# Performance work log

Hardware: AMD Instinct MI355X
Metric: run time of the kernel (lower is better)

Reference implementation:

```python
import jax, jax.numpy as jnp
import numpy as np

B, N, E = 4, 10000, 320000
IN_F, ATT_D, H = 256, 256, 8
DK = ATT_D // H  # 32
ALPHA = 0.2      # leaky relu slope
NORM_IDX = 0     # attention_norm_idx


def setup_inputs() -> dict:
    key = jax.random.key(0)
    k1, k2, k3, k4 = jax.random.split(key, 4)
    x = jax.random.normal(k1, (B, N, IN_F), dtype=jnp.float32)
    edge = jax.random.randint(k2, (B, 2, E), 0, N)
    # xavier_normal-ish init
    W = jax.random.normal(k3, (IN_F, ATT_D), dtype=jnp.float32) * (1.414 * np.sqrt(2.0 / (IN_F + ATT_D))).astype(np.float32)
    a = jax.random.normal(k4, (1, 2 * DK, 1, 1), dtype=jnp.float32) * 0.1
    return {"x": x, "edge": edge, "W": W, "a": a}


def reference(x, edge, W, a):
    # wx: [B, N, ATT_D]
    wx = jnp.einsum('bni,io->bno', x, W)
    # h: [B, N, DK, H] (view(B,-1,h,d_k).transpose(2,3))
    h = wx.reshape(B, N, H, DK).transpose(0, 1, 3, 2)
    # a * edge_h summed over the 2*DK dim is linear per endpoint, so
    # precompute per-node scores then gather per edge (same math, no [B,2dk,E,H] tensor).
    a_vec = a[0, :, 0, 0]            # [2*DK]
    a_src, a_dst = a_vec[:DK], a_vec[DK:]
    s_src = jnp.einsum('bnkh,k->bnh', h, a_src)   # [B, N, H]
    s_dst = jnp.einsum('bnkh,k->bnh', h, a_dst)   # [B, N, H]
    src = edge[:, 0, :]  # [B, E]
    dst = edge[:, 1, :]
    e_lin = (jnp.take_along_axis(s_src, src[:, :, None], axis=1)
             + jnp.take_along_axis(s_dst, dst[:, :, None], axis=1))  # [B, E, H]
    edge_e = jnp.where(e_lin >= 0, e_lin, ALPHA * e_lin)  # leaky relu
    # segment softmax grouped by edge[:, NORM_IDX, :], per batch element
    seg = (edge[:, NORM_IDX, :] + jnp.arange(B)[:, None] * N).reshape(-1)  # [B*E]
    scores = edge_e.reshape(B * E, H)
    mx = jax.ops.segment_max(scores, seg, num_segments=B * N)   # [B*N, H]
    ex = jnp.exp(scores - mx[seg])
    denom = jax.ops.segment_sum(ex, seg, num_segments=B * N)
    attention = (ex / (denom[seg] + 1e-16)).reshape(B, E, H)
    return attention, wx
```

## Files before the change

kernel.cpp:

```cpp
#include <hip/hip_runtime.h>
#include <hip/hip_bf16.h>

#define BB 4
#define NN 10000
#define EE 320000
#define HH 8
#define NHQ 2
#define NRQ 2
#define SEGR (NN / NRQ)
#define NSLICE 16
#define ESL (EE / NSLICE)
#define UU 4
#define SCALE 16777216.0f
#define INVSC (1.0f / 16777216.0f)

typedef float f4 __attribute__((ext_vector_type(4)));
typedef short s8v __attribute__((ext_vector_type(8)));
typedef unsigned short u16x8 __attribute__((ext_vector_type(8)));

__device__ __forceinline__ unsigned short f2bf(float f) {
  unsigned int u = __float_as_uint(f);
  u += 0x7FFFu + ((u >> 16) & 1u);
  return (unsigned short)(u >> 16);
}
__device__ __forceinline__ float bf2f(unsigned short s) {
  return __uint_as_float(((unsigned int)s) << 16);
}
__device__ __forceinline__ unsigned int ordf(float f) {
  unsigned int u = __float_as_uint(f);
  return (u & 0x80000000u) ? ~u : (u | 0x80000000u);
}
__device__ __forceinline__ float unordf(unsigned int u) {
  unsigned int b = (u & 0x80000000u) ? (u & 0x7FFFFFFFu) : ~u;
  return __uint_as_float(b);
}

__global__ __launch_bounds__(256) void k_transpose(const float* __restrict__ W,
                                                   unsigned short* __restrict__ Wt,
                                                   unsigned int* __restrict__ mxbuf) {
  if (blockIdx.x == 0 && blockIdx.y == 0 && threadIdx.x < 16) mxbuf[threadIdx.x] = 0u;
  __shared__ float tile[64][65];
  const int n0 = blockIdx.x * 64, k0 = blockIdx.y * 64;
  for (int i = threadIdx.x; i < 4096; i += 256) {
    int kk = i >> 6, nn = i & 63;
    tile[kk][nn] = W[(size_t)(k0 + kk) * 256 + n0 + nn];
  }
  __syncthreads();
  for (int i = threadIdx.x; i < 4096; i += 256) {
    int nn = i >> 6, kk = i & 63;
    Wt[(size_t)(n0 + nn) * 256 + (k0 + kk)] = f2bf(tile[kk][nn]);
  }
}

__global__ __launch_bounds__(256, 2) void k_gemm(const float* __restrict__ x,
                                                 const unsigned short* __restrict__ Wt,
                                                 const float* __restrict__ a,
                                                 float* __restrict__ wx,
                                                 unsigned short* __restrict__ ssbf,
                                                 unsigned short* __restrict__ sdbf,
                                                 unsigned int* __restrict__ mxbuf) {
  __shared__ unsigned short sA[64][40];
  __shared__ unsigned short sB[256][40];
  __shared__ unsigned int lmx[16];
  const int tid = threadIdx.x;
  const int lane = tid & 63;
  const int wv = tid >> 6;
  const int row0 = blockIdx.x << 6;
  const int fr = lane & 15;
  const int fg = lane >> 4;
  f4 acc[4][4] = {};
  const int ar = tid >> 2;
  const int ak = (tid & 3) << 3;
  if (tid < 16) lmx[tid] = 0u;

  for (int k0 = 0; k0 < 256; k0 += 32) {
    const float* xp = x + (size_t)(row0 + ar) * 256 + k0 + ak;
    f4 v0 = *(const f4*)xp;
    f4 v1 = *(const f4*)(xp + 4);
    u16x8 av;
    av[0] = f2bf(v0[0]); av[1] = f2bf(v0[1]); av[2] = f2bf(v0[2]); av[3] = f2bf(v0[3]);
    av[4] = f2bf(v1[0]); av[5] = f2bf(v1[1]); av[6] = f2bf(v1[2]); av[7] = f2bf(v1[3]);
    *(u16x8*)&sA[ar][ak] = av;
#pragma unroll
    for (int j = 0; j < 4; ++j) {
      int ci = tid + (j << 8);
      int col = ci >> 2;
      int ks = (ci & 3) << 3;
      *(u16x8*)&sB[col][ks] = *(const u16x8*)(Wt + (size_t)col * 256 + k0 + ks);
    }
    __syncthreads();
    s8v afr[4], bfr[4];
#pragma unroll
    for (int m = 0; m < 4; ++m) afr[m] = *(const s8v*)&sA[m * 16 + fr][fg << 3];
#pragma unroll
    for (int n = 0; n < 4; ++n) bfr[n] = *(const s8v*)&sB[wv * 64 + n * 16 + fr][fg << 3];
#pragma unroll
    for (int m = 0; m < 4; ++m)
#pragma unroll
      for (int n = 0; n < 4; ++n)
        acc[m][n] = __builtin_amdgcn_mfma_f32_16x16x32_bf16(afr[m], bfr[n], acc[m][n], 0, 0, 0);
    __syncthreads();
  }
#pragma unroll
  for (int m = 0; m < 4; ++m)
#pragma unroll
    for (int n = 0; n < 4; ++n) {
      int col = wv * 64 + n * 16 + fr;
#pragma unroll
      for (int q = 0; q < 4; ++q) {
        int row = row0 + m * 16 + fg * 4 + q;
        wx[(size_t)row * 256 + col] = acc[m][n][q];
      }
    }
  const float as0 = a[fr], as1 = a[16 + fr];
  const float ad0 = a[32 + fr], ad1 = a[48 + fr];
  unsigned mp0 = 0u, mp1 = 0u, md0 = 0u, md1 = 0u;
#pragma unroll
  for (int m = 0; m < 4; ++m)
#pragma unroll
    for (int q = 0; q < 4; ++q) {
      float p0 = acc[m][0][q] * as0 + acc[m][1][q] * as1;
      float p1 = acc[m][2][q] * as0 + acc[m][3][q] * as1;
      float d0 = acc[m][0][q] * ad0 + acc[m][1][q] * ad1;
      float d1 = acc[m][2][q] * ad0 + acc[m][3][q] * ad1;
#pragma unroll
      for (int msk = 1; msk <= 8; msk <<= 1) {
        p0 += __shfl_xor(p0, msk);
        p1 += __shfl_xor(p1, msk);
        d0 += __shfl_xor(d0, msk);
        d1 += __shfl_xor(d1, msk);
      }
      mp0 = max(mp0, ordf(p0)); mp1 = max(mp1, ordf(p1));
      md0 = max(md0, ordf(d0)); md1 = max(md1, ordf(d1));
      if (fr == 0) {
        int row = row0 + m * 16 + fg * 4 + q;
        unsigned sspk = (unsigned)f2bf(p0) | ((unsigned)f2bf(p1) << 16);
        unsigned sdpk = (unsigned)f2bf(d0) | ((unsigned)f2bf(d1) << 16);
        ((unsigned*)ssbf)[(size_t)row * 4 + wv] = sspk;
        ((unsigned*)sdbf)[(size_t)row * 4 + wv] = sdpk;
      }
    }
  if (fr == 0) {
    atomicMax(&lmx[wv * 2],     mp0);
    atomicMax(&lmx[wv * 2 + 1], mp1);
    atomicMax(&lmx[8 + wv * 2],     md0);
    atomicMax(&lmx[8 + wv * 2 + 1], md1);
  }
  __syncthreads();
  if (tid < 16 && lmx[tid]) atomicMax(&mxbuf[tid], lmx[tid]);
}

__global__ __launch_bounds__(1024) void k_bin(const int* __restrict__ edge,
                                              const unsigned short* __restrict__ ssbf,
                                              const unsigned short* __restrict__ sdbf,
                                              const unsigned int* __restrict__ mxbuf,
                                              unsigned int* __restrict__ partial) {
  extern __shared__ unsigned int ldsu[];
  unsigned int* hist = ldsu;
  uint2* stg = (uint2*)(ldsu + 4 * SEGR);
  const int blk = blockIdx.x;
  const int r = blk & (NSLICE - 1);
  const int c = blk / NSLICE;
  const int rq = c & 1;
  const int hq = (c >> 1) & 1;
  const int b = c >> 2;
  const int tid = threadIdx.x;
  const int lo = rq * SEGR;
  for (int i = tid; i < 4 * SEGR; i += 1024) hist[i] = 0u;
  const unsigned short* ssb = ssbf + ((size_t)b * NN + lo) * 8 + hq * 4;
  for (int i = tid; i < SEGR; i += 1024) stg[i] = *(const uint2*)(ssb + (size_t)i * 8);
  __syncthreads();
  float MH[4];
#pragma unroll
  for (int j = 0; j < 4; ++j)
    MH[j] = fmaxf(unordf(mxbuf[hq * 4 + j]) + unordf(mxbuf[8 + hq * 4 + j]), 0.f);
  const int* eps = edge + (size_t)b * 2 * EE + r * ESL;
  const int* epd = eps + EE;
  const unsigned short* sdb = sdbf + (size_t)b * NN * 8 + hq * 4;
  for (int base = 0; base < ESL; base += UU * 1024) {
    int ls4[UU], dst4[UU];
    bool v4[UU];
#pragma unroll
    for (int u = 0; u < UU; ++u) {
      int i = base + tid + u * 1024;
      bool inb = i < ESL;
      int s = inb ? eps[i] : 0;
      dst4[u] = inb ? epd[i] : 0;
      int ls = s - lo;
      v4[u] = inb && ((unsigned)ls < (unsigned)SEGR);
      ls4[u] = ls;
    }
    uint2 du4[UU];
#pragma unroll
    for (int u = 0; u < UU; ++u)
      if (v4[u]) du4[u] = *(const uint2*)(sdb + (size_t)dst4[u] * 8);
#pragma unroll
    for (int u = 0; u < UU; ++u) {
      if (v4[u]) {
        uint2 su = stg[ls4[u]];
        float t0 = __uint_as_float(su.x << 16) + __uint_as_float(du4[u].x << 16);
        float t1 = __uint_as_float(su.x & 0xFFFF0000u) + __uint_as_float(du4[u].x & 0xFFFF0000u);
        float t2 = __uint_as_float(su.y << 16) + __uint_as_float(du4[u].y << 16);
        float t3 = __uint_as_float(su.y & 0xFFFF0000u) + __uint_as_float(du4[u].y & 0xFFFF0000u);
        t0 = t0 >= 0.f ? t0 : 0.2f * t0;
        t1 = t1 >= 0.f ? t1 : 0.2f * t1;
        t2 = t2 >= 0.f ? t2 : 0.2f * t2;
        t3 = t3 >= 0.f ? t3 : 0.2f * t3;
        atomicAdd(&hist[0 * SEGR + ls4[u]], (unsigned)(__expf(t0 - MH[0]) * SCALE + 0.5f));
        atomicAdd(&hist[1 * SEGR + ls4[u]], (unsigned)(__expf(t1 - MH[1]) * SCALE + 0.5f));
        atomicAdd(&hist[2 * SEGR + ls4[u]], (unsigned)(__expf(t2 - MH[2]) * SCALE + 0.5f));
        atomicAdd(&hist[3 * SEGR + ls4[u]], (unsigned)(__expf(t3 - MH[3]) * SCALE + 0.5f));
      }
    }
  }
  __syncthreads();
  f4* pout = (f4*)(partial + (size_t)blk * (4 * SEGR));
  const f4* lin = (const f4*)hist;
  for (int i = tid; i < SEGR; i += 1024) pout[i] = lin[i];
}

__global__ __launch_bounds__(256) void k_reduce(const unsigned int* __restrict__ partial,
                                                unsigned short* __restrict__ dnbf) {
  const int t = blockIdx.x * 256 + threadIdx.x;
  if (t >= BB * NHQ * NRQ * SEGR) return;
  const int ls = t % SEGR;
  const int c = t / SEGR;
  const unsigned int* pp = partial + (size_t)c * NSLICE * (4 * SEGR);
  unsigned long long s[4] = {0, 0, 0, 0};
#pragma unroll 4
  for (int r = 0; r < NSLICE; ++r)
#pragma unroll
    for (int h = 0; h < 4; ++h)
      s[h] += pp[(size_t)r * (4 * SEGR) + h * SEGR + ls];
  const int rq = c & 1, hq = (c >> 1) & 1, b = c >> 2;
  uint2 pk;
  pk.x = (unsigned)f2bf((float)s[0] * INVSC) | ((unsigned)f2bf((float)s[1] * INVSC) << 16);
  pk.y = (unsigned)f2bf((float)s[2] * INVSC) | ((unsigned)f2bf((float)s[3] * INVSC) << 16);
  *(uint2*)(dnbf + ((size_t)b * NN + rq * SEGR + ls) * 8 + hq * 4) = pk;
}

__global__ __launch_bounds__(256) void k_fin(const int* __restrict__ edge,
                                             const unsigned short* __restrict__ ssbf,
                                             const unsigned short* __restrict__ sdbf,
                                             const unsigned short* __restrict__ dnbf,
                                             const unsigned int* __restrict__ mxbuf,
                                             float* __restrict__ att) {
  const int idx = blockIdx.x * 256 + threadIdx.x;
  const int b = idx / EE;
  const int e = idx - b * EE;
  const int src = edge[(size_t)b * 2 * EE + e];
  const int dst = edge[(size_t)b * 2 * EE + EE + e];
  const size_t seg = (size_t)b * NN + src;
  float MM[8];
#pragma unroll
  for (int j = 0; j < 8; ++j)
    MM[j] = fmaxf(unordf(mxbuf[j]) + unordf(mxbuf[8 + j]), 0.f);
  u16x8 ss = *(const u16x8*)(ssbf + seg * 8);
  u16x8 sd = *(const u16x8*)(sdbf + ((size_t)b * NN + dst) * 8);
  u16x8 dn = *(const u16x8*)(dnbf + seg * 8);
  f4 o0, o1;
#pragma unroll
  for (int j = 0; j < 4; ++j) {
    float t0 = bf2f(ss[j]) + bf2f(sd[j]);
    t0 = t0 >= 0.f ? t0 : 0.2f * t0;
    float t1 = bf2f(ss[4 + j]) + bf2f(sd[4 + j]);
    t1 = t1 >= 0.f ? t1 : 0.2f * t1;
    float n0 = __expf(t0 - MM[j]);
    float n1 = __expf(t1 - MM[4 + j]);
    o0[j] = n0 / fmaxf(bf2f(dn[j]), n0);
    o1[j] = n1 / fmaxf(bf2f(dn[4 + j]), n1);
  }
  f4* op = (f4*)(att + (size_t)idx * 8);
  op[0] = o0;
  op[1] = o1;
}

extern "C" void kernel_launch(void* const* d_in, const int* in_sizes, int n_in,
                              void* d_out, int out_size, void* d_ws, size_t ws_size,
                              hipStream_t stream) {
  const float* x = (const float*)d_in[0];
  const int* edge = (const int*)d_in[1];
  const float* W = (const float*)d_in[2];
  const float* a = (const float*)d_in[3];

  float* att = (float*)d_out;
  float* wx = att + (size_t)BB * EE * HH;

  unsigned int* partial = (unsigned int*)att;

  char* ws = (char*)d_ws;
  unsigned short* Wt = (unsigned short*)ws;
  unsigned short* ssbf = (unsigned short*)(ws + 131072);
  unsigned short* sdbf = ssbf + 320000;
  unsigned short* dnbf = sdbf + 320000;
  unsigned int* mxbuf = (unsigned int*)(dnbf + 320000);

  hipFuncSetAttribute((const void*)k_bin, hipFuncAttributeMaxDynamicSharedMemorySize,
                      4 * SEGR * 4 + SEGR * 8);

  k_transpose<<<dim3(4, 4), 256, 0, stream>>>(W, Wt, mxbuf);
  k_gemm<<<625, 256, 0, stream>>>(x, Wt, a, wx, ssbf, sdbf, mxbuf);
  k_bin<<<BB * NHQ * NRQ * NSLICE, 1024, 4 * SEGR * 4 + SEGR * 8, stream>>>(edge, ssbf, sdbf, mxbuf, partial);
  k_reduce<<<(BB * NHQ * NRQ * SEGR + 255) / 256, 256, 0, stream>>>(partial, dnbf);
  k_fin<<<5000, 256, 0, stream>>>(edge, ssbf, sdbf, dnbf, mxbuf, att);
}
```

Baseline: 89.78 us.

## Restructure GEMM: LDS-resident W half per block, per-wave 16-row strips with register A

Result: slower. 93.32 us (+3.9%).

```diff
diff --git a/kernel.cpp b/kernel.cpp
--- a/kernel.cpp
+++ b/kernel.cpp
@@ -52,99 +52,95 @@
   }
 }
 
-__global__ __launch_bounds__(256, 2) void k_gemm(const float* __restrict__ x,
+__global__ __launch_bounds__(512, 4) void k_gemm(const float* __restrict__ x,
                                                  const unsigned short* __restrict__ Wt,
                                                  const float* __restrict__ a,
                                                  float* __restrict__ wx,
                                                  unsigned short* __restrict__ ssbf,
                                                  unsigned short* __restrict__ sdbf,
                                                  unsigned int* __restrict__ mxbuf) {
-  __shared__ unsigned short sA[64][40];
-  __shared__ unsigned short sB[256][40];
-  __shared__ unsigned int lmx[16];
+  extern __shared__ char dyn[];
+  unsigned short (*sB)[256] = (unsigned short(*)[256])dyn;
+  unsigned int* lmx = (unsigned int*)(dyn + 128 * 256 * 2);
   const int tid = threadIdx.x;
+  const int wv = tid >> 6;
   const int lane = tid & 63;
-  const int wv = tid >> 6;
-  const int row0 = blockIdx.x << 6;
   const int fr = lane & 15;
   const int fg = lane >> 4;
-  f4 acc[4][4] = {};
-  const int ar = tid >> 2;
-  const int ak = (tid & 3) << 3;
+  const int ch = blockIdx.x & 1;
+  const int strip = (blockIdx.x >> 1) * 8 + wv;
   if (tid < 16) lmx[tid] = 0u;
-
-  for (int k0 = 0; k0 < 256; k0 += 32) {
-    const float* xp = x + (size_t)(row0 + ar) * 256 + k0 + ak;
-    f4 v0 = *(const f4*)xp;
-    f4 v1 = *(const f4*)(xp + 4);
-    u16x8 av;
-    av[0] = f2bf(v0[0]); av[1] = f2bf(v0[1]); av[2] = f2bf(v0[2]); av[3] = f2bf(v0[3]);
-    av[4] = f2bf(v1[0]); av[5] = f2bf(v1[1]); av[6] = f2bf(v1[2]); av[7] = f2bf(v1[3]);
-    *(u16x8*)&sA[ar][ak] = av;
+#pragma unroll
+  for (int p = 0; p < 8; ++p) {
+    int q = p * 512 + tid;
+    int c = q >> 5;
+    int kcc = q & 31;
+    *(u16x8*)&sB[c][(kcc ^ (c & 7)) << 3] =
+        *(const u16x8*)(Wt + (size_t)(ch * 128 + c) * 256 + (kcc << 3));
+  }
+  __syncthreads();
+  if (strip < 2500) {
+    const float* ap = x + (size_t)(strip * 16 + fr) * 256 + (fg << 3);
+    f4 v0 = *(const f4*)ap;
+    f4 v1 = *(const f4*)(ap + 4);
+    f4 acc[8] = {};
+    const int sw = fr & 7;
+#pragma unroll
+    for (int k0 = 0; k0 < 256; k0 += 32) {
+      u16x8 av;
+      av[0] = f2bf(v0[0]); av[1] = f2bf(v0[1]); av[2] = f2bf(v0[2]); av[3] = f2bf(v0[3]);
+      av[4] = f2bf(v1[0]); av[5] = f2bf(v1[1]); av[6] = f2bf(v1[2]); av[7] = f2bf(v1[3]);
+      s8v afr = *(s8v*)&av;
+      if (k0 < 224) {
+        v0 = *(const f4*)(ap + k0 + 32);
+        v1 = *(const f4*)(ap + k0 + 36);
+      }
+      const int kb = k0 >> 3;
+#pragma unroll
+      for (int n = 0; n < 8; ++n) {
+        s8v bfr = *(const s8v*)&sB[n * 16 + fr][((kb + fg) ^ sw) << 3];
+        acc[n] = __builtin_amdgcn_mfma_f32_16x16x32_bf16(afr, bfr, acc[n], 0, 0, 0);
+      }
+    }
+    const size_t rb = (size_t)strip * 16;
+#pragma unroll
+    for (int n = 0; n < 8; ++n) {
+      int col = ch * 128 + n * 16 + fr;
+#pragma unroll
+      for (int q = 0; q < 4; ++q)
+        wx[(rb + fg * 4 + q) * 256 + col] = acc[n][q];
+    }
+    const float as0 = a[fr], as1 = a[16 + fr];
+    const float ad0 = a[32 + fr], ad1 = a[48 + fr];
 #pragma unroll
     for (int j = 0; j < 4; ++j) {
-      int ci = tid + (j << 8);
-      int col = ci >> 2;
-      int ks = (ci & 3) << 3;
-      *(u16x8*)&sB[col][ks] = *(const u16x8*)(Wt + (size_t)col * 256 + k0 + ks);
-    }
-    __syncthreads();
-    s8v afr[4], bfr[4];
-#pragma unroll
-    for (int m = 0; m < 4; ++m) afr[m] = *(const s8v*)&sA[m * 16 + fr][fg << 3];
-#pragma unroll
-    for (int n = 0; n < 4; ++n) bfr[n] = *(const s8v*)&sB[wv * 64 + n * 16 + fr][fg << 3];
-#pragma unroll
-    for (int m = 0; m < 4; ++m)
-#pragma unroll
-      for (int n = 0; n < 4; ++n)
-        acc[m][n] = __builtin_amdgcn_mfma_f32_16x16x32_bf16(afr[m], bfr[n], acc[m][n], 0, 0, 0);
-    __syncthreads();
-  }
-#pragma unroll
-  for (int m = 0; m < 4; ++m)
-#pragma unroll
-    for (int n = 0; n < 4; ++n) {
-      int col = wv * 64 + n * 16 + fr;
+      unsigned mp = 0u, md = 0u;
 #pragma unroll
       for (int q = 0; q < 4; ++q) {
-        int row = row0 + m * 16 + fg * 4 + q;
-        wx[(size_t)row * 256 + col] = acc[m][n][q];
-      }
-    }
-  const float as0 = a[fr], as1 = a[16 + fr];
-  const float ad0 = a[32 + fr], ad1 = a[48 + fr];
-  unsigned mp0 = 0u, mp1 = 0u, md0 = 0u, md1 = 0u;
-#pragma unroll
-  for (int m = 0; m < 4; ++m)
-#pragma unroll
-    for (int q = 0; q < 4; ++q) {
-      float p0 = acc[m][0][q] * as0 + acc[m][1][q] * as1;
-      float p1 = acc[m][2][q] * as0 + acc[m][3][q] * as1;
-      float d0 = acc[m][0][q] * ad0 + acc[m][1][q] * ad1;
-      float d1 = acc[m][2][q] * ad0 + acc[m][3][q] * ad1;
-#pragma unroll
-      for (int msk = 1; msk <= 8; msk <<= 1) {
-        p0 += __shfl_xor(p0, msk);
-        p1 += __shfl_xor(p1, msk);
-        d0 += __shfl_xor(d0, msk);
-        d1 += __shfl_xor(d1, msk);
-      }
-      mp0 = max(mp0, ordf(p0)); mp1 = max(mp1, ordf(p1));
-      md0 = max(md0, ordf(d0)); md1 = max(md1, ordf(d1));
-      if (fr == 0) {
-        int row = row0 + m * 16 + fg * 4 + q;
-        unsigned sspk = (unsigned)f2bf(p0) | ((unsigned)f2bf(p1) << 16);
-        unsigned sdpk = (unsigned)f2bf(d0) | ((unsigned)f2bf(d1) << 16);
-        ((unsigned*)ssbf)[(size_t)row * 4 + wv] = sspk;
-        ((unsigned*)sdbf)[(size_t)row * 4 + wv] = sdpk;
-      }
-    }
-  if (fr == 0) {
-    atomicMax(&lmx[wv * 2],     mp0);
-    atomicMax(&lmx[wv * 2 + 1], mp1);
-    atomicMax(&lmx[8 + wv * 2],     md0);
-    atomicMax(&lmx[8 + wv * 2 + 1], md1);
+        float p = acc[2 * j][q] * as0 + acc[2 * j + 1][q] * as1;
+        float d = acc[2 * j][q] * ad0 + acc[2 * j + 1][q] * ad1;
+#pragma unroll
+        for (int m = 1; m <= 8; m <<= 1) {
+          p += __shfl_xor(p, m);
+          d += __shfl_xor(d, m);
+        }
+        mp = max(mp, ordf(p));
+        md = max(md, ordf(d));
+        if (fr == 0) {
+          size_t row = rb + fg * 4 + q;
+          ssbf[row * 8 + ch * 4 + j] = f2bf(p);
+          sdbf[row * 8 + ch * 4 + j] = f2bf(d);
+        }
+      }
+      mp = max(mp, (unsigned)__shfl_xor((int)mp, 16));
+      mp = max(mp, (unsigned)__shfl_xor((int)mp, 32));
+      md = max(md, (unsigned)__shfl_xor((int)md, 16));
+      md = max(md, (unsigned)__shfl_xor((int)md, 32));
+      if (lane == 0) {
+        atomicMax(&lmx[ch * 4 + j], mp);
+        atomicMax(&lmx[8 + ch * 4 + j], md);
+      }
+    }
   }
   __syncthreads();
   if (tid < 16 && lmx[tid]) atomicMax(&mxbuf[tid], lmx[tid]);
@@ -295,11 +291,13 @@
   unsigned short* dnbf = sdbf + 320000;
   unsigned int* mxbuf = (unsigned int*)(dnbf + 320000);
 
+  const int gemmLds = 128 * 256 * 2 + 64;
+  hipFuncSetAttribute((const void*)k_gemm, hipFuncAttributeMaxDynamicSharedMemorySize, gemmLds);
   hipFuncSetAttribute((const void*)k_bin, hipFuncAttributeMaxDynamicSharedMemorySize,
                       4 * SEGR * 4 + SEGR * 8);
 
   k_transpose<<<dim3(4, 4), 256, 0, stream>>>(W, Wt, mxbuf);
-  k_gemm<<<625, 256, 0, stream>>>(x, Wt, a, wx, ssbf, sdbf, mxbuf);
+  k_gemm<<<626, 512, gemmLds, stream>>>(x, Wt, a, wx, ssbf, sdbf, mxbuf);
   k_bin<<<BB * NHQ * NRQ * NSLICE, 1024, 4 * SEGR * 4 + SEGR * 8, stream>>>(edge, ssbf, sdbf, mxbuf, partial);
   k_reduce<<<(BB * NHQ * NRQ * SEGR + 255) / 256, 256, 0, stream>>>(partial, dnbf);
   k_fin<<<5000, 256, 0, stream>>>(edge, ssbf, sdbf, dnbf, mxbuf, att);
```

## Pre-convert x to bf16 and stream GEMM tiles via direct global-to-LDS loads

Applied to the files above, without the earlier changes.

Measured after the change: 93.96 us. 4.7% more time.

```diff
diff --git a/kernel.cpp b/kernel.cpp
--- a/kernel.cpp
+++ b/kernel.cpp
@@ -34,6 +34,10 @@
   unsigned int b = (u & 0x80000000u) ? (u & 0x7FFFFFFFu) : ~u;
   return __uint_as_float(b);
 }
+__device__ __forceinline__ void gload_lds16(const void* g, void* l) {
+  __builtin_amdgcn_global_load_lds((const __attribute__((address_space(1))) void*)g,
+                                   (__attribute__((address_space(3))) void*)l, 16, 0, 0);
+}
 
 __global__ __launch_bounds__(256) void k_transpose(const float* __restrict__ W,
                                                    unsigned short* __restrict__ Wt,
@@ -52,48 +56,60 @@
   }
 }
 
-__global__ __launch_bounds__(256, 2) void k_gemm(const float* __restrict__ x,
+__global__ __launch_bounds__(512) void k_cvt2(const float* __restrict__ x,
+                                              unsigned short* __restrict__ xbf) {
+  const int t = blockIdx.x * 512 + threadIdx.x;
+  const f4* in = (const f4*)(x + (size_t)t * 8);
+  f4 v0 = in[0], v1 = in[1];
+  u16x8 o;
+  o[0] = f2bf(v0[0]); o[1] = f2bf(v0[1]); o[2] = f2bf(v0[2]); o[3] = f2bf(v0[3]);
+  o[4] = f2bf(v1[0]); o[5] = f2bf(v1[1]); o[6] = f2bf(v1[2]); o[7] = f2bf(v1[3]);
+  *(u16x8*)(xbf + (size_t)t * 8) = o;
+}
+
+__global__ __launch_bounds__(256, 4) void k_gemm(const unsigned short* __restrict__ xbf,
                                                  const unsigned short* __restrict__ Wt,
                                                  const float* __restrict__ a,
                                                  float* __restrict__ wx,
                                                  unsigned short* __restrict__ ssbf,
                                                  unsigned short* __restrict__ sdbf,
                                                  unsigned int* __restrict__ mxbuf) {
-  __shared__ unsigned short sA[64][40];
-  __shared__ unsigned short sB[256][40];
+  __shared__ unsigned short sA[64 * 32];
+  __shared__ unsigned short sB[256 * 32];
   __shared__ unsigned int lmx[16];
   const int tid = threadIdx.x;
+  const int wv = tid >> 6;
   const int lane = tid & 63;
-  const int wv = tid >> 6;
-  const int row0 = blockIdx.x << 6;
   const int fr = lane & 15;
   const int fg = lane >> 4;
+  const int row0 = blockIdx.x << 6;
+  if (tid < 16) lmx[tid] = 0u;
   f4 acc[4][4] = {};
-  const int ar = tid >> 2;
-  const int ak = (tid & 3) << 3;
-  if (tid < 16) lmx[tid] = 0u;
+
+  const int arow = tid >> 2, ac = tid & 3;
+  const int acg = ac ^ ((arow ^ (arow >> 2)) & 3);
+  const unsigned short* agp = xbf + (size_t)(row0 + arow) * 256 + acg * 8;
+  const unsigned short* bgp[4];
+#pragma unroll
+  for (int p = 0; p < 4; ++p) {
+    int s = p * 256 + tid;
+    int col = s >> 2, c = s & 3;
+    int cg = c ^ ((col ^ (col >> 2)) & 3);
+    bgp[p] = Wt + (size_t)col * 256 + cg * 8;
+  }
+  const int frag_off = (fg ^ ((fr ^ (fr >> 2)) & 3)) << 3;
 
   for (int k0 = 0; k0 < 256; k0 += 32) {
-    const float* xp = x + (size_t)(row0 + ar) * 256 + k0 + ak;
-    f4 v0 = *(const f4*)xp;
-    f4 v1 = *(const f4*)(xp + 4);
-    u16x8 av;
-    av[0] = f2bf(v0[0]); av[1] = f2bf(v0[1]); av[2] = f2bf(v0[2]); av[3] = f2bf(v0[3]);
-    av[4] = f2bf(v1[0]); av[5] = f2bf(v1[1]); av[6] = f2bf(v1[2]); av[7] = f2bf(v1[3]);
-    *(u16x8*)&sA[ar][ak] = av;
-#pragma unroll
-    for (int j = 0; j < 4; ++j) {
-      int ci = tid + (j << 8);
-      int col = ci >> 2;
-      int ks = (ci & 3) << 3;
-      *(u16x8*)&sB[col][ks] = *(const u16x8*)(Wt + (size_t)col * 256 + k0 + ks);
-    }
+    gload_lds16(agp + k0, sA + (wv << 9));
+#pragma unroll
+    for (int p = 0; p < 4; ++p)
+      gload_lds16(bgp[p] + k0, sB + p * 2048 + (wv << 9));
     __syncthreads();
     s8v afr[4], bfr[4];
 #pragma unroll
-    for (int m = 0; m < 4; ++m) afr[m] = *(const s8v*)&sA[m * 16 + fr][fg << 3];
-#pragma unroll
-    for (int n = 0; n < 4; ++n) bfr[n] = *(const s8v*)&sB[wv * 64 + n * 16 + fr][fg << 3];
+    for (int m = 0; m < 4; ++m) afr[m] = *(const s8v*)&sA[(m * 16 + fr) * 32 + frag_off];
+#pragma unroll
+    for (int n = 0; n < 4; ++n) bfr[n] = *(const s8v*)&sB[(wv * 64 + n * 16 + fr) * 32 + frag_off];
 #pragma unroll
     for (int m = 0; m < 4; ++m)
 #pragma unroll
@@ -286,6 +302,7 @@
   float* att = (float*)d_out;
   float* wx = att + (size_t)BB * EE * HH;
 
+  unsigned short* xbf = (unsigned short*)(att + 5120000);
   unsigned int* partial = (unsigned int*)att;
 
   char* ws = (char*)d_ws;
@@ -299,7 +316,8 @@
                       4 * SEGR * 4 + SEGR * 8);
 
   k_transpose<<<dim3(4, 4), 256, 0, stream>>>(W, Wt, mxbuf);
-  k_gemm<<<625, 256, 0, stream>>>(x, Wt, a, wx, ssbf, sdbf, mxbuf);
+  k_cvt2<<<2500, 512, 0, stream>>>(x, xbf);
+  k_gemm<<<625, 256, 0, stream>>>(xbf, Wt, a, wx, ssbf, sdbf, mxbuf);
   k_bin<<<BB * NHQ * NRQ * NSLICE, 1024, 4 * SEGR * 4 + SEGR * 8, stream>>>(edge, ssbf, sdbf, mxbuf, partial);
   k_reduce<<<(BB * NHQ * NRQ * SEGR + 255) / 256, 256, 0, stream>>>(partial, dnbf);
   k_fin<<<5000, 256, 0, stream>>>(edge, ssbf, sdbf, dnbf, mxbuf, att);
```
